# Performance work log

Measured on AMD Instinct MI355X. Metric: run time of the kernel, lower is better.

## Reference

```python
import jax, jax.numpy as jnp
import numpy as np

N_USERS = 200000
N_ITEMS = 100000
N_NODES = N_USERS + N_ITEMS
EMBED_DIM = 64
N_LAYERS = 3
N_EDGES = 5000000
BATCH = 4096


def setup_inputs() -> dict:
    key = jax.random.key(0)
    ks = jax.random.split(key, 8)
    # Xavier-uniform-ish init for embedding tables
    lim = float(np.sqrt(6.0 / (N_USERS + EMBED_DIM)))
    user_emb = jax.random.uniform(ks[0], (N_USERS, EMBED_DIM), jnp.float32, -lim, lim)
    lim_i = float(np.sqrt(6.0 / (N_ITEMS + EMBED_DIM)))
    item_emb = jax.random.uniform(ks[1], (N_ITEMS, EMBED_DIM), jnp.float32, -lim_i, lim_i)
    # sparse normalized adjacency in COO form (values ~ 1/sqrt(du*di), use small positives)
    adj_vals = jax.random.uniform(ks[2], (N_EDGES,), jnp.float32, 0.0, 0.1)
    adj_rows = jax.random.randint(ks[3], (N_EDGES,), 0, N_NODES, jnp.int32)
    adj_cols = jax.random.randint(ks[4], (N_EDGES,), 0, N_NODES, jnp.int32)
    users = jax.random.randint(ks[5], (BATCH,), 0, N_USERS, jnp.int32)
    pos_items = jax.random.randint(ks[6], (BATCH,), 0, N_ITEMS, jnp.int32)
    neg_items = jax.random.randint(ks[7], (BATCH,), 0, N_ITEMS, jnp.int32)
    return {
        "user_emb": user_emb, "item_emb": item_emb, "adj_vals": adj_vals,
        "adj_rows": adj_rows, "adj_cols": adj_cols,
        "users": users, "pos_items": pos_items, "neg_items": neg_items,
    }


def _spmm(adj_rows, adj_cols, adj_vals, x):
    # y = A @ x for sparse COO A: gather source rows, scale, scatter-add to dest rows
    msgs = adj_vals[:, None] * x[adj_cols]          # [n_edges, d]
    return jax.ops.segment_sum(msgs, adj_rows, num_segments=N_NODES)


def reference(user_emb, item_emb, adj_vals, adj_rows, adj_cols, users, pos_items, neg_items):
    # E^0 = concat(user, item); E^k = A @ E^{k-1}; final = mean over k=0..K
    E = jnp.concatenate([user_emb, item_emb], axis=0)   # [N_NODES, d]
    acc = E
    cur = E
    for _ in range(N_LAYERS):
        cur = _spmm(adj_rows, adj_cols, adj_vals, cur)
        acc = acc + cur
    E_final = acc / jnp.asarray(N_LAYERS + 1, E.dtype)
    e_u = E_final[users]                         # users index into user block
    e_pos = E_final[N_USERS + pos_items]         # items offset by n_users
    e_neg = E_final[N_USERS + neg_items]
    return jnp.stack([e_u, e_pos, e_neg], axis=0)  # [3, B, d]
```

## Files before the change

### kernel.cpp

```cpp
#include <hip/hip_runtime.h>
#include <hip/hip_fp16.h>
#include <stdint.h>

#define N_USERS   200000
#define N_ITEMS   100000
#define N_NODES   300000
#define EMBED_DIM 64
#define N_EDGES   5000000
#define BATCH     4096

#define ROWS_PER_BUCKET 512
#define PART_K 586
#define PART_B 1024
#define CHUNK  4884
#define PART_L (PART_K * PART_B)
#define SCAN_T 1024
#define SCAN_NB (PART_L / SCAN_T)

#define VAL_SCALE 81920.0f
#define VAL_INV   (1.0f / 81920.0f)
#define FIN_CAP   10240

#define EMB_SCALE 1024.0f
#define EMB_INV   (1.0f / 1024.0f)

typedef float f32x2 __attribute__((ext_vector_type(2)));

__device__ __forceinline__ int swz(int b)     { return ((b & 7) << 7) | (b >> 3); }

__global__ void part_count(const int* __restrict__ rows, int* __restrict__ hist) {
    __shared__ int h[PART_K];
    for (int i = threadIdx.x; i < PART_K; i += blockDim.x) h[i] = 0;
    __syncthreads();
    int beg = blockIdx.x * CHUNK;
    int end = min(beg + CHUNK, N_EDGES);
    for (int i = beg + (int)threadIdx.x * 4; i < end; i += blockDim.x * 4) {
        int4 r4 = *(const int4*)(rows + i);
        atomicAdd(&h[r4.x >> 9], 1);
        atomicAdd(&h[r4.y >> 9], 1);
        atomicAdd(&h[r4.z >> 9], 1);
        atomicAdd(&h[r4.w >> 9], 1);
    }
    __syncthreads();
    for (int i = threadIdx.x; i < PART_K; i += blockDim.x)
        hist[blockIdx.x * PART_K + i] = h[i];
}

__global__ void scan_partial(const int* __restrict__ hist,
                             int* __restrict__ local_scan,
                             int* __restrict__ block_sums) {
    __shared__ int sh[SCAN_T];
    int tid = threadIdx.x;
    int gid = blockIdx.x * SCAN_T + tid;
    int p = gid & (PART_B - 1);
    int k = gid >> 10;
    int b = ((p & 127) << 3) | (p >> 7);
    int v = hist[b * PART_K + k];
    sh[tid] = v;
    __syncthreads();
    for (int off = 1; off < SCAN_T; off <<= 1) {
        int t = (tid >= off) ? sh[tid - off] : 0;
        __syncthreads();
        sh[tid] += t;
        __syncthreads();
    }
    local_scan[gid] = sh[tid] - v;
    if (tid == SCAN_T - 1) block_sums[blockIdx.x] = sh[tid];
}

__global__ void scan_addoff(const int* __restrict__ local_scan,
                            const int* __restrict__ block_sums,
                            int* __restrict__ sofs,
                            int* __restrict__ row_ptr) {
    __shared__ int sh[1024];
    int tid = threadIdx.x;
    int v = (tid < SCAN_NB) ? block_sums[tid] : 0;
    sh[tid] = v;
    __syncthreads();
    for (int off = 1; off < 1024; off <<= 1) {
        int t = (tid >= off) ? sh[tid - off] : 0;
        __syncthreads();
        sh[tid] += t;
        __syncthreads();
    }
    int base = (blockIdx.x == 0) ? 0 : sh[blockIdx.x - 1];
    int gid = blockIdx.x * SCAN_T + tid;
    sofs[gid] = local_scan[gid] + base;
    if (gid == 0) row_ptr[N_NODES] = N_EDGES;
}

__global__ void part_scatter(const int* __restrict__ rows,
                             const int* __restrict__ cols,
                             const float* __restrict__ vals,
                             const int* __restrict__ sofs,
                             unsigned int* __restrict__ ppay,
                             unsigned short* __restrict__ prloc) {
    __shared__ int lcnt[PART_K];
    __shared__ int lbase[PART_K];
    __shared__ int gbase[PART_K];
    __shared__ int sc[1024];
    __shared__ unsigned int   pay[CHUNK];
    __shared__ unsigned short rl[CHUNK];
    __shared__ unsigned short bk[CHUNK];
    int b = blockIdx.x;
    int tid = threadIdx.x;
    int myp = swz(b);
    for (int i = tid; i < PART_K; i += 1024) {
        lcnt[i] = 0;
        gbase[i] = sofs[i * PART_B + myp];
    }
    __syncthreads();
    int beg = b * CHUNK;
    int end = min(beg + CHUNK, N_EDGES);
    int n = end - beg;
    for (int i = beg + tid * 4; i < end; i += 4096) {
        int4 r4 = *(const int4*)(rows + i);
        atomicAdd(&lcnt[r4.x >> 9], 1);
        atomicAdd(&lcnt[r4.y >> 9], 1);
        atomicAdd(&lcnt[r4.z >> 9], 1);
        atomicAdd(&lcnt[r4.w >> 9], 1);
    }
    __syncthreads();
    int v = (tid < PART_K) ? lcnt[tid] : 0;
    sc[tid] = v;
    __syncthreads();
    for (int off = 1; off < 1024; off <<= 1) {
        int t = (tid >= off) ? sc[tid - off] : 0;
        __syncthreads();
        sc[tid] += t;
        __syncthreads();
    }
    if (tid < PART_K) {
        int excl = sc[tid] - v;
        lbase[tid] = excl;
        lcnt[tid] = excl;
    }
    __syncthreads();
    for (int i = beg + tid * 4; i < end; i += 4096) {
        int4 r4 = *(const int4*)(rows + i);
        int4 c4 = *(const int4*)(cols + i);
        float4 v4 = *(const float4*)(vals + i);
        int rr[4] = {r4.x, r4.y, r4.z, r4.w};
        int cc[4] = {c4.x, c4.y, c4.z, c4.w};
        float vv[4] = {v4.x, v4.y, v4.z, v4.w};
        #pragma unroll
        for (int j = 0; j < 4; ++j) {
            int r = rr[j];
            int k = r >> 9;
            int p = atomicAdd(&lcnt[k], 1);
            unsigned int q = (unsigned int)min(8191, (int)(vv[j] * VAL_SCALE + 0.5f));
            pay[p] = (unsigned int)cc[j] | (q << 19);
            rl[p] = (unsigned short)(r & 511);
            bk[p] = (unsigned short)k;
        }
    }
    __syncthreads();
    for (int i = tid; i < n; i += 1024) {
        int k = bk[i];
        int a = gbase[k] + (i - lbase[k]);
        ppay[a] = pay[i];
        prloc[a] = rl[i];
    }
}

__global__ void csr_finalize(const unsigned int* __restrict__ ppay,
                             const unsigned short* __restrict__ prloc,
                             const int* __restrict__ sofs,
                             int* __restrict__ row_ptr,
                             unsigned int* __restrict__ sorted) {
    __shared__ int cnt[ROWS_PER_BUCKET];
    __shared__ int cur[ROWS_PER_BUCKET];
    __shared__ int sc[ROWS_PER_BUCKET];
    __shared__ unsigned int obuf[FIN_CAP];
    int k = blockIdx.x;
    int tid = threadIdx.x;
    int seg_beg = sofs[k * PART_B];
    int seg_end = (k + 1 < PART_K) ? sofs[(k + 1) * PART_B] : N_EDGES;
    int n = seg_end - seg_beg;

    cnt[tid] = 0;
    __syncthreads();
    for (int i = seg_beg + tid; i < seg_end; i += ROWS_PER_BUCKET)
        atomicAdd(&cnt[prloc[i]], 1);
    __syncthreads();

    int v = cnt[tid];
    sc[tid] = v;
    __syncthreads();
    for (int off = 1; off < 512; off <<= 1) {
        int t = (tid >= off) ? sc[tid - off] : 0;
        __syncthreads();
        sc[tid] += t;
        __syncthreads();
    }
    int excl = sc[tid] - v;

    int row = k * ROWS_PER_BUCKET + tid;
    if (row < N_NODES) row_ptr[row] = seg_beg + excl;
    cur[tid] = excl;
    __syncthreads();

    if (n <= FIN_CAP) {
        for (int i = seg_beg + tid; i < seg_end; i += ROWS_PER_BUCKET) {
            int r = prloc[i];
            int lp = atomicAdd(&cur[r], 1);
            obuf[lp] = ppay[i];
        }
        __syncthreads();
        for (int i = tid; i < n; i += ROWS_PER_BUCKET)
            sorted[seg_beg + i] = obuf[i];
    } else {
        for (int i = seg_beg + tid; i < seg_end; i += ROWS_PER_BUCKET) {
            int r = prloc[i];
            int lp = atomicAdd(&cur[r], 1);
            sorted[seg_beg + lp] = ppay[i];
        }
    }
}

__global__ void convert_emb(const float* __restrict__ ue,
                            const float* __restrict__ ie,
                            uint2* __restrict__ xf8) {
    int t = blockIdx.x * blockDim.x + threadIdx.x;
    if (t >= N_NODES * 8) return;
    int flat = t * 8;
    int row = flat >> 6;
    int off = flat & 63;
    const float* src = (row < N_USERS) ? (ue + (size_t)row * 64 + off)
                                       : (ie + (size_t)(row - N_USERS) * 64 + off);
    float4 a = ((const float4*)src)[0];
    float4 b = ((const float4*)src)[1];
    int lo = __builtin_amdgcn_cvt_pk_fp8_f32(a.x * EMB_SCALE, a.y * EMB_SCALE, 0, 0);
    lo     = __builtin_amdgcn_cvt_pk_fp8_f32(a.z * EMB_SCALE, a.w * EMB_SCALE, lo, 1);
    int hi = __builtin_amdgcn_cvt_pk_fp8_f32(b.x * EMB_SCALE, b.y * EMB_SCALE, 0, 0);
    hi     = __builtin_amdgcn_cvt_pk_fp8_f32(b.z * EMB_SCALE, b.w * EMB_SCALE, hi, 1);
    xf8[t] = make_uint2((unsigned int)lo, (unsigned int)hi);
}

#define ACCF8A(vv, u, A) { \
    f32x2 g0_ = __builtin_amdgcn_cvt_pk_f32_fp8((int)(u).x, 0); \
    f32x2 g1_ = __builtin_amdgcn_cvt_pk_f32_fp8((int)(u).x, 1); \
    f32x2 g2_ = __builtin_amdgcn_cvt_pk_f32_fp8((int)(u).y, 0); \
    f32x2 g3_ = __builtin_amdgcn_cvt_pk_f32_fp8((int)(u).y, 1); \
    A[0] += (vv) * g0_.x; A[1] += (vv) * g0_.y; \
    A[2] += (vv) * g1_.x; A[3] += (vv) * g1_.y; \
    A[4] += (vv) * g2_.x; A[5] += (vv) * g2_.y; \
    A[6] += (vv) * g3_.x; A[7] += (vv) * g3_.y; }

#define ACCHA(vv, r, A) { \
    const __half2* hp_ = (const __half2*)&(r); \
    float2 f0_ = __half22float2(hp_[0]); \
    float2 f1_ = __half22float2(hp_[1]); \
    float2 f2_ = __half22float2(hp_[2]); \
    float2 f3_ = __half22float2(hp_[3]); \
    A[0] += (vv) * f0_.x; A[1] += (vv) * f0_.y; \
    A[2] += (vv) * f1_.x; A[3] += (vv) * f1_.y; \
    A[4] += (vv) * f2_.x; A[5] += (vv) * f2_.y; \
    A[6] += (vv) * f3_.x; A[7] += (vv) * f3_.y; }

__global__ __launch_bounds__(256, 6)
void spmm_f8f8(const int* __restrict__ row_ptr,
               const unsigned int* __restrict__ sorted,
               const uint2* __restrict__ xf8,
               uint2* __restrict__ yf8) {
    int t = blockIdx.x * blockDim.x + threadIdx.x;
    int row = t >> 3;
    int l8 = t & 7;
    if (row >= N_NODES) return;
    int beg = row_ptr[row];
    int end = row_ptr[row + 1];
    float acc[8] = {0.f, 0.f, 0.f, 0.f, 0.f, 0.f, 0.f, 0.f};
    int e = beg;
    for (; e + 8 <= end; e += 8) {
        unsigned int cv[8];
        #pragma unroll
        for (int j = 0; j < 8; ++j) cv[j] = sorted[e + j];
        uint2 r[8];
        #pragma unroll
        for (int j = 0; j < 8; ++j)
            r[j] = xf8[(size_t)(cv[j] & 0x7FFFF) * 8 + l8];
        #pragma unroll
        for (int j = 0; j < 8; ++j) {
            float v = (float)(cv[j] >> 19) * VAL_INV;
            ACCF8A(v, r[j], acc);
        }
    }
    for (; e + 4 <= end; e += 4) {
        unsigned int cv[4];
        #pragma unroll
        for (int j = 0; j < 4; ++j) cv[j] = sorted[e + j];
        uint2 r[4];
        #pragma unroll
        for (int j = 0; j < 4; ++j)
            r[j] = xf8[(size_t)(cv[j] & 0x7FFFF) * 8 + l8];
        #pragma unroll
        for (int j = 0; j < 4; ++j) {
            float v = (float)(cv[j] >> 19) * VAL_INV;
            ACCF8A(v, r[j], acc);
        }
    }
    for (; e < end; ++e) {
        unsigned int cv = sorted[e];
        uint2 r0 = xf8[(size_t)(cv & 0x7FFFF) * 8 + l8];
        float v = (float)(cv >> 19) * VAL_INV;
        ACCF8A(v, r0, acc);
    }
    int lo = __builtin_amdgcn_cvt_pk_fp8_f32(acc[0], acc[1], 0, 0);
    lo     = __builtin_amdgcn_cvt_pk_fp8_f32(acc[2], acc[3], lo, 1);
    int hi = __builtin_amdgcn_cvt_pk_fp8_f32(acc[4], acc[5], 0, 0);
    hi     = __builtin_amdgcn_cvt_pk_fp8_f32(acc[6], acc[7], hi, 1);
    yf8[(size_t)row * 8 + l8] = make_uint2((unsigned int)lo, (unsigned int)hi);
}

__global__ __launch_bounds__(256, 6)
void spmm_f8f16(const int* __restrict__ row_ptr,
                const unsigned int* __restrict__ sorted,
                const uint2* __restrict__ xf8,
                __half* __restrict__ yh) {
    int t = blockIdx.x * blockDim.x + threadIdx.x;
    int row = t >> 3;
    int l8 = t & 7;
    if (row >= N_NODES) return;
    int beg = row_ptr[row];
    int end = row_ptr[row + 1];
    float acc[8] = {0.f, 0.f, 0.f, 0.f, 0.f, 0.f, 0.f, 0.f};
    int e = beg;
    for (; e + 8 <= end; e += 8) {
        unsigned int cv[8];
        #pragma unroll
        for (int j = 0; j < 8; ++j) cv[j] = sorted[e + j];
        uint2 r[8];
        #pragma unroll
        for (int j = 0; j < 8; ++j)
            r[j] = xf8[(size_t)(cv[j] & 0x7FFFF) * 8 + l8];
        #pragma unroll
        for (int j = 0; j < 8; ++j) {
            float v = (float)(cv[j] >> 19) * VAL_INV;
            ACCF8A(v, r[j], acc);
        }
    }
    for (; e + 4 <= end; e += 4) {
        unsigned int cv[4];
        #pragma unroll
        for (int j = 0; j < 4; ++j) cv[j] = sorted[e + j];
        uint2 r[4];
        #pragma unroll
        for (int j = 0; j < 4; ++j)
            r[j] = xf8[(size_t)(cv[j] & 0x7FFFF) * 8 + l8];
        #pragma unroll
        for (int j = 0; j < 4; ++j) {
            float v = (float)(cv[j] >> 19) * VAL_INV;
            ACCF8A(v, r[j], acc);
        }
    }
    for (; e < end; ++e) {
        unsigned int cv = sorted[e];
        uint2 r0 = xf8[(size_t)(cv & 0x7FFFF) * 8 + l8];
        float v = (float)(cv >> 19) * VAL_INV;
        ACCF8A(v, r0, acc);
    }
    float4 ov;
    ((__half2*)&ov)[0] = __floats2half2_rn(acc[0], acc[1]);
    ((__half2*)&ov)[1] = __floats2half2_rn(acc[2], acc[3]);
    ((__half2*)&ov)[2] = __floats2half2_rn(acc[4], acc[5]);
    ((__half2*)&ov)[3] = __floats2half2_rn(acc[6], acc[7]);
    ((float4*)yh)[(size_t)row * 8 + l8] = ov;
}

__global__ __launch_bounds__(256, 4)
void final_kernel(const int* __restrict__ row_ptr,
                  const unsigned int* __restrict__ sorted,
                  const float* __restrict__ user_emb,
                  const float* __restrict__ item_emb,
                  const uint2* __restrict__ x0f8,
                  const __half* __restrict__ E2h,
                  const int* __restrict__ users,
                  const int* __restrict__ pos_items,
                  const int* __restrict__ neg_items,
                  float* __restrict__ out) {
    int t = blockIdx.x * blockDim.x + threadIdx.x;
    int slot = t >> 3;
    int l8 = t & 7;
    if (slot >= 3 * BATCH) return;
    int which = slot >> 12;
    int idx   = slot & (BATCH - 1);
    int node;
    if (which == 0)      node = users[idx];
    else if (which == 1) node = N_USERS + pos_items[idx];
    else                 node = N_USERS + neg_items[idx];

    const float4* e2v = (const float4*)E2h;

    float a1[8] = {0.f, 0.f, 0.f, 0.f, 0.f, 0.f, 0.f, 0.f};
    float a3[8] = {0.f, 0.f, 0.f, 0.f, 0.f, 0.f, 0.f, 0.f};
    int beg = row_ptr[node];
    int end = row_ptr[node + 1];
    int e = beg;
    for (; e + 4 <= end; e += 4) {
        unsigned int cv[4];
        #pragma unroll
        for (int j = 0; j < 4; ++j) cv[j] = sorted[e + j];
        uint2 rx[4];
        float4 r2[4];
        #pragma unroll
        for (int j = 0; j < 4; ++j) {
            size_t col = (size_t)(cv[j] & 0x7FFFF);
            rx[j] = x0f8[col * 8 + l8];
            r2[j] = e2v[col * 8 + l8];
        }
        #pragma unroll
        for (int j = 0; j < 4; ++j) {
            float v = (float)(cv[j] >> 19) * VAL_INV;
            ACCF8A(v, rx[j], a1);
            ACCHA(v, r2[j], a3);
        }
    }
    for (; e < end; ++e) {
        unsigned int cv = sorted[e];
        size_t col = (size_t)(cv & 0x7FFFF);
        uint2 rx = x0f8[col * 8 + l8];
        float4 r2 = e2v[col * 8 + l8];
        float v = (float)(cv >> 19) * VAL_INV;
        ACCF8A(v, rx, a1);
        ACCHA(v, r2, a3);
    }

    const float* t0 = (node < N_USERS) ? (user_emb + (size_t)node * 64)
                                       : (item_emb + (size_t)(node - N_USERS) * 64);
    float4 e0a = ((const float4*)t0)[l8 * 2];
    float4 e0b = ((const float4*)t0)[l8 * 2 + 1];

    float4 e2c = e2v[(size_t)node * 8 + l8];
    const __half2* h2 = (const __half2*)&e2c;
    float e2[8];
    {
        float2 b0 = __half22float2(h2[0]), b1 = __half22float2(h2[1]);
        float2 b2 = __half22float2(h2[2]), b3 = __half22float2(h2[3]);
        e2[0]=b0.x; e2[1]=b0.y; e2[2]=b1.x; e2[3]=b1.y;
        e2[4]=b2.x; e2[5]=b2.y; e2[6]=b3.x; e2[7]=b3.y;
    }
    float4 ra, rb;
    ra.x = (e0a.x + (a1[0] + e2[0] + a3[0]) * EMB_INV) * 0.25f;
    ra.y = (e0a.y + (a1[1] + e2[1] + a3[1]) * EMB_INV) * 0.25f;
    ra.z = (e0a.z + (a1[2] + e2[2] + a3[2]) * EMB_INV) * 0.25f;
    ra.w = (e0a.w + (a1[3] + e2[3] + a3[3]) * EMB_INV) * 0.25f;
    rb.x = (e0b.x + (a1[4] + e2[4] + a3[4]) * EMB_INV) * 0.25f;
    rb.y = (e0b.y + (a1[5] + e2[5] + a3[5]) * EMB_INV) * 0.25f;
    rb.z = (e0b.z + (a1[6] + e2[6] + a3[6]) * EMB_INV) * 0.25f;
    rb.w = (e0b.w + (a1[7] + e2[7] + a3[7]) * EMB_INV) * 0.25f;
    ((float4*)out)[(size_t)slot * 16 + l8 * 2]     = ra;
    ((float4*)out)[(size_t)slot * 16 + l8 * 2 + 1] = rb;
}

extern "C" void kernel_launch(void* const* d_in, const int* in_sizes, int n_in,
                              void* d_out, int out_size, void* d_ws, size_t ws_size,
                              hipStream_t stream) {
    const float* user_emb  = (const float*)d_in[0];
    const float* item_emb  = (const float*)d_in[1];
    const float* adj_vals  = (const float*)d_in[2];
    const int*   adj_rows  = (const int*)d_in[3];
    const int*   adj_cols  = (const int*)d_in[4];
    const int*   users     = (const int*)d_in[5];
    const int*   pos_items = (const int*)d_in[6];
    const int*   neg_items = (const int*)d_in[7];
    float* out = (float*)d_out;

    char* ws = (char*)d_ws;
    size_t off = 0;
    auto alloc = [&](size_t bytes) -> void* {
        void* p = ws + off;
        off = (off + bytes + 255) & ~(size_t)255;
        return p;
    };
    int*  hist       = (int*) alloc((size_t)(PART_L + 32) * sizeof(int));
    int*  local_scan = (int*) alloc((size_t)(PART_L + 32) * sizeof(int));
    int*  sofs       = (int*) alloc((size_t)(PART_L + 32) * sizeof(int));
    int*  block_sums = (int*) alloc((size_t)(SCAN_NB + 32) * sizeof(int));
    int*  row_ptr    = (int*) alloc((size_t)(N_NODES + 32) * sizeof(int));
    unsigned int*   ppay  = (unsigned int*)  alloc((size_t)N_EDGES * sizeof(unsigned int));
    unsigned short* prloc = (unsigned short*)alloc((size_t)N_EDGES * sizeof(unsigned short));
    unsigned int* sorted = (unsigned int*)alloc((size_t)N_EDGES * sizeof(unsigned int));
    uint2*  x0f8 = (uint2*) alloc((size_t)N_NODES * EMBED_DIM);
    uint2*  E1f8 = (uint2*) alloc((size_t)N_NODES * EMBED_DIM);
    __half* E2h  = (__half*)alloc((size_t)N_NODES * EMBED_DIM * sizeof(__half));

    part_count<<<PART_B, 1024, 0, stream>>>(adj_rows, hist);
    scan_partial<<<SCAN_NB, SCAN_T, 0, stream>>>(hist, local_scan, block_sums);
    scan_addoff<<<SCAN_NB, SCAN_T, 0, stream>>>(local_scan, block_sums, sofs, row_ptr);
    part_scatter<<<PART_B, 1024, 0, stream>>>(adj_rows, adj_cols, adj_vals, sofs, ppay, prloc);
    csr_finalize<<<PART_K, ROWS_PER_BUCKET, 0, stream>>>(ppay, prloc, sofs, row_ptr, sorted);

    const int TB = 256;
    convert_emb<<<(N_NODES * 8 + TB - 1) / TB, TB, 0, stream>>>(user_emb, item_emb, x0f8);

    int spmm_blocks = (N_NODES * 8 + TB - 1) / TB;
    spmm_f8f8 <<<spmm_blocks, TB, 0, stream>>>(row_ptr, sorted, x0f8, E1f8);
    spmm_f8f16<<<spmm_blocks, TB, 0, stream>>>(row_ptr, sorted, E1f8, E2h);

    int final_blocks = (3 * BATCH * 8 + TB - 1) / TB;
    final_kernel<<<final_blocks, TB, 0, stream>>>(
        row_ptr, sorted, user_emb, item_emb, x0f8, E2h, users, pos_items, neg_items, out);
}
```

Baseline: 394.3 us.

## Reuse per-chunk histogram in scatter and store batch E1 rows during first SpMM

part_scatter now seeds its per-bucket counts from the histogram part_count already computed, so it no longer re-reads the rows and redoes the shared-memory atomics. A bitmap of batch nodes is built, and the first SpMM also writes fp16 E1 rows for those nodes. The final kernel then reads E1 directly instead of recomputing A·x0 over neighbours. The final kernel also splits each node's edge loop across two 8-lane groups and combines them with a shuffle. This adds two small kernels, a bitmap check in every SpMM thread and an extra fp16 buffer.

```diff
diff --git a/kernel.cpp b/kernel.cpp
--- a/kernel.cpp
+++ b/kernel.cpp
@@ -20,6 +20,8 @@
 #define VAL_SCALE 81920.0f
 #define VAL_INV   (1.0f / 81920.0f)
 #define FIN_CAP   10240
+
+#define BM_WORDS  ((N_NODES + 31) / 32)
 
 #define EMB_SCALE 1024.0f
 #define EMB_INV   (1.0f / 1024.0f)
@@ -44,6 +46,26 @@
     __syncthreads();
     for (int i = threadIdx.x; i < PART_K; i += blockDim.x)
         hist[blockIdx.x * PART_K + i] = h[i];
+}
+
+__global__ void bm_zero(unsigned int* __restrict__ bm) {
+    int t = blockIdx.x * blockDim.x + threadIdx.x;
+    if (t < BM_WORDS) bm[t] = 0u;
+}
+
+__global__ void bm_mark(const int* __restrict__ users,
+                        const int* __restrict__ pos_items,
+                        const int* __restrict__ neg_items,
+                        unsigned int* __restrict__ bm) {
+    int t = blockIdx.x * blockDim.x + threadIdx.x;
+    if (t >= 3 * BATCH) return;
+    int which = t >> 12;
+    int idx   = t & (BATCH - 1);
+    int node;
+    if (which == 0)      node = users[idx];
+    else if (which == 1) node = N_USERS + pos_items[idx];
+    else                 node = N_USERS + neg_items[idx];
+    atomicOr(&bm[node >> 5], 1u << (node & 31));
 }
 
 __global__ void scan_partial(const int* __restrict__ hist,
@@ -92,6 +114,7 @@
 __global__ void part_scatter(const int* __restrict__ rows,
                              const int* __restrict__ cols,
                              const float* __restrict__ vals,
+                             const int* __restrict__ hist,
                              const int* __restrict__ sofs,
                              unsigned int* __restrict__ ppay,
                              unsigned short* __restrict__ prloc) {
@@ -106,21 +129,13 @@
     int tid = threadIdx.x;
     int myp = swz(b);
     for (int i = tid; i < PART_K; i += 1024) {
-        lcnt[i] = 0;
+        lcnt[i] = hist[b * PART_K + i];
         gbase[i] = sofs[i * PART_B + myp];
     }
     __syncthreads();
     int beg = b * CHUNK;
     int end = min(beg + CHUNK, N_EDGES);
     int n = end - beg;
-    for (int i = beg + tid * 4; i < end; i += 4096) {
-        int4 r4 = *(const int4*)(rows + i);
-        atomicAdd(&lcnt[r4.x >> 9], 1);
-        atomicAdd(&lcnt[r4.y >> 9], 1);
-        atomicAdd(&lcnt[r4.z >> 9], 1);
-        atomicAdd(&lcnt[r4.w >> 9], 1);
-    }
-    __syncthreads();
     int v = (tid < PART_K) ? lcnt[tid] : 0;
     sc[tid] = v;
     __syncthreads();
@@ -262,7 +277,9 @@
 void spmm_f8f8(const int* __restrict__ row_ptr,
                const unsigned int* __restrict__ sorted,
                const uint2* __restrict__ xf8,
-               uint2* __restrict__ yf8) {
+               const unsigned int* __restrict__ bm,
+               uint2* __restrict__ yf8,
+               __half* __restrict__ yh_batch) {
     int t = blockIdx.x * blockDim.x + threadIdx.x;
     int row = t >> 3;
     int l8 = t & 7;
@@ -310,6 +327,14 @@
     int hi = __builtin_amdgcn_cvt_pk_fp8_f32(acc[4], acc[5], 0, 0);
     hi     = __builtin_amdgcn_cvt_pk_fp8_f32(acc[6], acc[7], hi, 1);
     yf8[(size_t)row * 8 + l8] = make_uint2((unsigned int)lo, (unsigned int)hi);
+    if ((bm[row >> 5] >> (row & 31)) & 1u) {
+        float4 ov;
+        ((__half2*)&ov)[0] = __floats2half2_rn(acc[0], acc[1]);
+        ((__half2*)&ov)[1] = __floats2half2_rn(acc[2], acc[3]);
+        ((__half2*)&ov)[2] = __floats2half2_rn(acc[4], acc[5]);
+        ((__half2*)&ov)[3] = __floats2half2_rn(acc[6], acc[7]);
+        ((float4*)yh_batch)[(size_t)row * 8 + l8] = ov;
+    }
 }
 
 __global__ __launch_bounds__(256, 6)
@@ -372,15 +397,16 @@
                   const unsigned int* __restrict__ sorted,
                   const float* __restrict__ user_emb,
                   const float* __restrict__ item_emb,
-                  const uint2* __restrict__ x0f8,
+                  const __half* __restrict__ E1h,
                   const __half* __restrict__ E2h,
                   const int* __restrict__ users,
                   const int* __restrict__ pos_items,
                   const int* __restrict__ neg_items,
                   float* __restrict__ out) {
     int t = blockIdx.x * blockDim.x + threadIdx.x;
-    int slot = t >> 3;
-    int l8 = t & 7;
+    int slot = t >> 4;
+    int sub  = (t >> 3) & 1;
+    int l8   = t & 7;
     if (slot >= 3 * BATCH) return;
     int which = slot >> 12;
     int idx   = slot & (BATCH - 1);
@@ -391,63 +417,66 @@
 
     const float4* e2v = (const float4*)E2h;
 
-    float a1[8] = {0.f, 0.f, 0.f, 0.f, 0.f, 0.f, 0.f, 0.f};
     float a3[8] = {0.f, 0.f, 0.f, 0.f, 0.f, 0.f, 0.f, 0.f};
     int beg = row_ptr[node];
     int end = row_ptr[node + 1];
-    int e = beg;
-    for (; e + 4 <= end; e += 4) {
+    int nq = (end - beg) >> 2;
+    for (int q = sub; q < nq; q += 2) {
+        int e = beg + (q << 2);
         unsigned int cv[4];
         #pragma unroll
         for (int j = 0; j < 4; ++j) cv[j] = sorted[e + j];
-        uint2 rx[4];
         float4 r2[4];
         #pragma unroll
-        for (int j = 0; j < 4; ++j) {
-            size_t col = (size_t)(cv[j] & 0x7FFFF);
-            rx[j] = x0f8[col * 8 + l8];
-            r2[j] = e2v[col * 8 + l8];
-        }
+        for (int j = 0; j < 4; ++j)
+            r2[j] = e2v[(size_t)(cv[j] & 0x7FFFF) * 8 + l8];
         #pragma unroll
         for (int j = 0; j < 4; ++j) {
             float v = (float)(cv[j] >> 19) * VAL_INV;
-            ACCF8A(v, rx[j], a1);
             ACCHA(v, r2[j], a3);
         }
     }
-    for (; e < end; ++e) {
-        unsigned int cv = sorted[e];
-        size_t col = (size_t)(cv & 0x7FFFF);
-        uint2 rx = x0f8[col * 8 + l8];
-        float4 r2 = e2v[col * 8 + l8];
-        float v = (float)(cv >> 19) * VAL_INV;
-        ACCF8A(v, rx, a1);
-        ACCHA(v, r2, a3);
-    }
+    if (sub == 0) {
+        for (int e = beg + (nq << 2); e < end; ++e) {
+            unsigned int cv = sorted[e];
+            float4 r2 = e2v[(size_t)(cv & 0x7FFFF) * 8 + l8];
+            float v = (float)(cv >> 19) * VAL_INV;
+            ACCHA(v, r2, a3);
+        }
+    }
+    #pragma unroll
+    for (int i = 0; i < 8; ++i) a3[i] += __shfl_xor(a3[i], 8);
+    if (sub) return;
 
     const float* t0 = (node < N_USERS) ? (user_emb + (size_t)node * 64)
                                        : (item_emb + (size_t)(node - N_USERS) * 64);
     float4 e0a = ((const float4*)t0)[l8 * 2];
     float4 e0b = ((const float4*)t0)[l8 * 2 + 1];
 
+    float4 e1c = ((const float4*)E1h)[(size_t)node * 8 + l8];
     float4 e2c = e2v[(size_t)node * 8 + l8];
+    const __half2* h1 = (const __half2*)&e1c;
     const __half2* h2 = (const __half2*)&e2c;
-    float e2[8];
+    float e1[8], e2[8];
     {
+        float2 a0 = __half22float2(h1[0]), a1 = __half22float2(h1[1]);
+        float2 a2 = __half22float2(h1[2]), a3h = __half22float2(h1[3]);
+        e1[0]=a0.x; e1[1]=a0.y; e1[2]=a1.x; e1[3]=a1.y;
+        e1[4]=a2.x; e1[5]=a2.y; e1[6]=a3h.x; e1[7]=a3h.y;
         float2 b0 = __half22float2(h2[0]), b1 = __half22float2(h2[1]);
         float2 b2 = __half22float2(h2[2]), b3 = __half22float2(h2[3]);
         e2[0]=b0.x; e2[1]=b0.y; e2[2]=b1.x; e2[3]=b1.y;
         e2[4]=b2.x; e2[5]=b2.y; e2[6]=b3.x; e2[7]=b3.y;
     }
     float4 ra, rb;
-    ra.x = (e0a.x + (a1[0] + e2[0] + a3[0]) * EMB_INV) * 0.25f;
-    ra.y = (e0a.y + (a1[1] + e2[1] + a3[1]) * EMB_INV) * 0.25f;
-    ra.z = (e0a.z + (a1[2] + e2[2] + a3[2]) * EMB_INV) * 0.25f;
-    ra.w = (e0a.w + (a1[3] + e2[3] + a3[3]) * EMB_INV) * 0.25f;
-    rb.x = (e0b.x + (a1[4] + e2[4] + a3[4]) * EMB_INV) * 0.25f;
-    rb.y = (e0b.y + (a1[5] + e2[5] + a3[5]) * EMB_INV) * 0.25f;
-    rb.z = (e0b.z + (a1[6] + e2[6] + a3[6]) * EMB_INV) * 0.25f;
-    rb.w = (e0b.w + (a1[7] + e2[7] + a3[7]) * EMB_INV) * 0.25f;
+    ra.x = (e0a.x + (e1[0] + e2[0] + a3[0]) * EMB_INV) * 0.25f;
+    ra.y = (e0a.y + (e1[1] + e2[1] + a3[1]) * EMB_INV) * 0.25f;
+    ra.z = (e0a.z + (e1[2] + e2[2] + a3[2]) * EMB_INV) * 0.25f;
+    ra.w = (e0a.w + (e1[3] + e2[3] + a3[3]) * EMB_INV) * 0.25f;
+    rb.x = (e0b.x + (e1[4] + e2[4] + a3[4]) * EMB_INV) * 0.25f;
+    rb.y = (e0b.y + (e1[5] + e2[5] + a3[5]) * EMB_INV) * 0.25f;
+    rb.z = (e0b.z + (e1[6] + e2[6] + a3[6]) * EMB_INV) * 0.25f;
+    rb.w = (e0b.w + (e1[7] + e2[7] + a3[7]) * EMB_INV) * 0.25f;
     ((float4*)out)[(size_t)slot * 16 + l8 * 2]     = ra;
     ((float4*)out)[(size_t)slot * 16 + l8 * 2 + 1] = rb;
 }
@@ -482,22 +511,27 @@
     unsigned int* sorted = (unsigned int*)alloc((size_t)N_EDGES * sizeof(unsigned int));
     uint2*  x0f8 = (uint2*) alloc((size_t)N_NODES * EMBED_DIM);
     uint2*  E1f8 = (uint2*) alloc((size_t)N_NODES * EMBED_DIM);
+    __half* E1h  = (__half*)alloc((size_t)N_NODES * EMBED_DIM * sizeof(__half));
     __half* E2h  = (__half*)alloc((size_t)N_NODES * EMBED_DIM * sizeof(__half));
+    unsigned int* bm = (unsigned int*)alloc((size_t)(BM_WORDS + 32) * sizeof(unsigned int));
+
+    const int TB = 256;
 
     part_count<<<PART_B, 1024, 0, stream>>>(adj_rows, hist);
+    bm_zero<<<(BM_WORDS + TB - 1) / TB, TB, 0, stream>>>(bm);
+    bm_mark<<<(3 * BATCH + TB - 1) / TB, TB, 0, stream>>>(users, pos_items, neg_items, bm);
     scan_partial<<<SCAN_NB, SCAN_T, 0, stream>>>(hist, local_scan, block_sums);
     scan_addoff<<<SCAN_NB, SCAN_T, 0, stream>>>(local_scan, block_sums, sofs, row_ptr);
-    part_scatter<<<PART_B, 1024, 0, stream>>>(adj_rows, adj_cols, adj_vals, sofs, ppay, prloc);
+    part_scatter<<<PART_B, 1024, 0, stream>>>(adj_rows, adj_cols, adj_vals, hist, sofs, ppay, prloc);
     csr_finalize<<<PART_K, ROWS_PER_BUCKET, 0, stream>>>(ppay, prloc, sofs, row_ptr, sorted);
 
-    const int TB = 256;
     convert_emb<<<(N_NODES * 8 + TB - 1) / TB, TB, 0, stream>>>(user_emb, item_emb, x0f8);
 
     int spmm_blocks = (N_NODES * 8 + TB - 1) / TB;
-    spmm_f8f8 <<<spmm_blocks, TB, 0, stream>>>(row_ptr, sorted, x0f8, E1f8);
+    spmm_f8f8 <<<spmm_blocks, TB, 0, stream>>>(row_ptr, sorted, x0f8, bm, E1f8, E1h);
     spmm_f8f16<<<spmm_blocks, TB, 0, stream>>>(row_ptr, sorted, E1f8, E2h);
 
-    int final_blocks = (3 * BATCH * 8 + TB - 1) / TB;
+    int final_blocks = (3 * BATCH * 16 + TB - 1) / TB;
     final_kernel<<<final_blocks, TB, 0, stream>>>(
-        row_ptr, sorted, user_emb, item_emb, x0f8, E2h, users, pos_items, neg_items, out);
-}
+        row_ptr, sorted, user_emb, item_emb, E1h, E2h, users, pos_items, neg_items, out);
+}
```

Result: slower. 612.9 us (+55.4%).
